# Kernel optimization log

Measured on AMD Instinct MI355X. Metric: run time of the kernel, lower is better.

Reference implementation:

```python
import jax, jax.numpy as jnp
import numpy as np

WH, WW = 7, 7           # window height/width
N = WH * WW             # tokens per window = 49
C = 768                 # num_channels
H = 24                  # num_heads
D = C // H              # head_dim = 32
B = 1024                # total windows (batch * windows-per-image)
NW = 64                 # windows per image (shift_mask leading dim)
EPS = 1e-5


def _relative_position_index():
    # Mirrors the torch buffer construction in __init__.
    coords = np.stack(np.meshgrid(np.arange(WH), np.arange(WW), indexing='ij'))  # [2,WH,WW]
    cf = coords.reshape(2, -1)                          # [2,N]
    rel = cf[:, :, None] - cf[:, None, :]               # [2,N,N]
    rel = rel.transpose(1, 2, 0).copy()                 # [N,N,2]
    rel[:, :, 0] += WH - 1
    rel[:, :, 1] += WW - 1
    rel[:, :, 0] *= 2 * WW - 1
    return jnp.asarray(rel.sum(-1), dtype=jnp.int32)    # [N,N]


def setup_inputs() -> dict:
    key = jax.random.key(0)
    ks = jax.random.split(key, 6)
    x = jax.random.normal(ks[0], (B, N, C), dtype=jnp.float32)
    shift_mask = jax.random.normal(ks[1], (NW, N, N), dtype=jnp.float32)
    w_qkv = jax.random.normal(ks[2], (3 * C, C), dtype=jnp.float32) * 0.02
    b_qkv = jnp.zeros((3 * C,), dtype=jnp.float32)
    w_proj = jax.random.normal(ks[3], (C, C), dtype=jnp.float32) * 0.02
    b_proj = jnp.zeros((C,), dtype=jnp.float32)
    rel_bias_table = jax.random.normal(ks[4], ((2 * WH - 1) * (2 * WW - 1), H), dtype=jnp.float32) * 0.02
    ln_g = jnp.ones((C,), dtype=jnp.float32)
    ln_b = jnp.zeros((C,), dtype=jnp.float32)
    rel_pos_index = _relative_position_index()
    return {
        'x': x, 'shift_mask': shift_mask,
        'w_qkv': w_qkv, 'b_qkv': b_qkv,
        'w_proj': w_proj, 'b_proj': b_proj,
        'rel_bias_table': rel_bias_table,
        'ln_g': ln_g, 'ln_b': ln_b,
        'rel_pos_index': rel_pos_index,
    }


def reference(x, shift_mask, w_qkv, b_qkv, w_proj, b_proj, rel_bias_table, ln_g, ln_b, rel_pos_index):
    B_, N_, C_ = x.shape
    # QKV projection: [B,N,3C] -> [3,B,H,N,D]
    qkv = (x @ w_qkv.T + b_qkv).reshape(B_, N_, 3, H, D).transpose(2, 0, 3, 1, 4)
    q, k, v = qkv[0], qkv[1], qkv[2]
    # Relative position bias gather: [N,N,H] -> [1,H,N,N]
    bias = rel_bias_table[rel_pos_index.reshape(-1)].reshape(N_, N_, H).transpose(2, 0, 1)[None]
    # Shift mask broadcast over batch repeats and heads: [B,1,N,N]
    mask = jnp.tile(shift_mask, (B_ // shift_mask.shape[0], 1, 1))[:, None]
    attn_bias = bias + mask  # [B,H,N,N]
    scale = 1.0 / np.sqrt(D).astype(np.float32)
    scores = jnp.einsum('bhnd,bhmd->bhnm', q, k) * scale + attn_bias
    attn = jax.nn.softmax(scores, axis=-1)
    out = jnp.einsum('bhnm,bhmd->bhnd', attn, v)       # [B,H,N,D]
    out = out.transpose(0, 2, 1, 3).reshape(B_, N_, C_)
    out = out @ w_proj.T + b_proj                      # dropout p=0 -> identity
    y = out + x
    mu = jnp.mean(y, axis=-1, keepdims=True)
    var = jnp.mean(jnp.square(y - mu), axis=-1, keepdims=True)
    return (y - mu) * jax.lax.rsqrt(var + EPS) * ln_g + ln_b
```

## Files before the change

### kernel.cpp

```cpp
#include <hip/hip_runtime.h>
#include <hip/hip_bf16.h>

#define SEQ 49
#define CH 768
#define NH 24
#define HD 32
#define NB 1024
#define NWIN 64
#define MTOT (NB*SEQ)

typedef __hip_bfloat16 bf16;
typedef __attribute__((ext_vector_type(8))) short short8;
typedef __attribute__((ext_vector_type(4))) short short4v;
typedef __attribute__((ext_vector_type(4))) float f32x4;

#define MD  ((size_t)MTOT * HD)
#define NHMD ((size_t)NH * MD)

__device__ __forceinline__ void gload16(const void* g, void* l) {
  __builtin_amdgcn_global_load_lds((__attribute__((address_space(1))) void*)g,
                                   (__attribute__((address_space(3))) void*)l,
                                   16, 0, 0);
}

__device__ __forceinline__ float bf2f(short s) {
  return __uint_as_float(((unsigned int)(unsigned short)s) << 16);
}

__global__ void cvt_bf16(const float* __restrict__ in, bf16* __restrict__ o, int n4) {
  int i = blockIdx.x * blockDim.x + threadIdx.x;
  if (i >= n4) return;
  float4 v = ((const float4*)in)[i];
  union { bf16 b[4]; short4 s; } u;
  u.b[0] = __float2bfloat16(v.x);
  u.b[1] = __float2bfloat16(v.y);
  u.b[2] = __float2bfloat16(v.z);
  u.b[3] = __float2bfloat16(v.w);
  ((short4*)o)[i] = u.s;
}

__global__ void build_comb(const float* __restrict__ table, const int* __restrict__ rpi,
                           const float* __restrict__ smask, bf16* __restrict__ comb) {
  int i = blockIdx.x * blockDim.x + threadIdx.x;
  if (i >= NWIN * NH * 1024) return;
  int idx = i * 4;
  int e0 = idx & 7;
  int l = (idx >> 3) & 63;
  int jj = (idx >> 9) & 7;
  int sh = idx >> 12;
  int h = sh % NH;
  int s = sh / NH;
  union { bf16 b[4]; short4 v; } u;
#pragma unroll
  for (int k = 0; k < 4; k++) {
    int j = jj * 8 + e0 + k;
    int mt = j >> 4, nt = (j >> 2) & 3, r = j & 3;
    int m = 16 * mt + 4 * (l >> 4) + r;
    int n = 16 * nt + (l & 15);
    float v = -1e30f;
    if (m < SEQ && n < SEQ)
      v = table[rpi[m * SEQ + n] * NH + h] + smask[s * SEQ * SEQ + m * SEQ + n];
    u.b[k] = __float2bfloat16(v);
  }
  *(short4*)(comb + idx) = u.v;
}

__global__ __launch_bounds__(512) void qkv_gemm(
    const bf16* __restrict__ A, const bf16* __restrict__ Bw,
    const float* __restrict__ bias, bf16* __restrict__ C)
{
  extern __shared__ __align__(16) bf16 lds[];
  const int tid = threadIdx.x;
  const int w = tid >> 6, l = tid & 63;
  const int lr = l & 15, lg = l >> 4;
  const int wm = w >> 2, wn = w & 3;

  const int flat = blockIdx.x;
  const int xcd = flat & 7, lid = flat >> 3;
  const int wgid = (xcd < 4 ? xcd * 221 : 884 + (xcd - 4) * 220) + lid;
  const int bm = wgid / 9, bn = wgid - 9 * bm;

  const bf16* gA[4];
  const bf16* gB[4];
  int ldst[4];
#pragma unroll
  for (int j = 0; j < 4; j++) {
    int c = j * 512 + tid;
    int row = c >> 3, cpos = c & 7;
    int srcch = cpos ^ (row & 7);
    gA[j] = A + ((size_t)(bm * 256 + row)) * CH + srcch * 8;
    gB[j] = Bw + ((size_t)(bn * 256 + row)) * CH + srcch * 8;
    ldst[j] = c * 8;
  }

  f32x4 acc[8][4];
  f32x4 zero4 = {0.f, 0.f, 0.f, 0.f};
#pragma unroll
  for (int i = 0; i < 8; i++)
#pragma unroll
    for (int j = 0; j < 4; j++) acc[i][j] = zero4;

  int offA[8][2], offB[4][2];
#pragma unroll
  for (int mi = 0; mi < 8; mi++)
#pragma unroll
    for (int ks = 0; ks < 2; ks++) {
      int rowa = wm * 128 + mi * 16 + lr;
      offA[mi][ks] = rowa * 64 + ((lg + 4 * ks) ^ (rowa & 7)) * 8;
    }
#pragma unroll
  for (int nj = 0; nj < 4; nj++)
#pragma unroll
    for (int ks = 0; ks < 2; ks++) {
      int rowb = wn * 64 + nj * 16 + lr;
      offB[nj][ks] = rowb * 64 + ((lg + 4 * ks) ^ (rowb & 7)) * 8;
    }

#pragma unroll
  for (int j = 0; j < 4; j++) gload16(gA[j], lds + ldst[j]);
#pragma unroll
  for (int j = 0; j < 4; j++) gload16(gB[j], lds + 32768 + ldst[j]);

  for (int t = 0; t < 12; ++t) {
    const int cur = t & 1;
    if (t < 11) {
      const int kk = (t + 1) * 64;
      bf16* nA = lds + (cur ^ 1) * 16384;
      bf16* nB = lds + 32768 + (cur ^ 1) * 16384;
#pragma unroll
      for (int j = 0; j < 4; j++) gload16(gA[j] + kk, nA + ldst[j]);
#pragma unroll
      for (int j = 0; j < 4; j++) gload16(gB[j] + kk, nB + ldst[j]);
      asm volatile("s_waitcnt vmcnt(8)" ::: "memory");
    } else {
      asm volatile("s_waitcnt vmcnt(0)" ::: "memory");
    }
    __builtin_amdgcn_sched_barrier(0);
    __builtin_amdgcn_s_barrier();
    __builtin_amdgcn_sched_barrier(0);
    const bf16* cA = lds + cur * 16384;
    const bf16* cB = lds + 32768 + cur * 16384;
#pragma unroll
    for (int ks = 0; ks < 2; ks++) {
      short8 af[8], bfv[4];
#pragma unroll
      for (int mi = 0; mi < 8; mi++) af[mi] = *(const short8*)(cA + offA[mi][ks]);
#pragma unroll
      for (int nj = 0; nj < 4; nj++) bfv[nj] = *(const short8*)(cB + offB[nj][ks]);
      __builtin_amdgcn_s_setprio(1);
#pragma unroll
      for (int mi = 0; mi < 8; mi++)
#pragma unroll
        for (int nj = 0; nj < 4; nj++)
          acc[mi][nj] = __builtin_amdgcn_mfma_f32_16x16x32_bf16(af[mi], bfv[nj], acc[mi][nj], 0, 0, 0);
      __builtin_amdgcn_s_setprio(0);
    }
    asm volatile("s_waitcnt lgkmcnt(0)" ::: "memory");
    __builtin_amdgcn_sched_barrier(0);
    __builtin_amdgcn_s_barrier();
    __builtin_amdgcn_sched_barrier(0);
  }

  const float scale = 0.17677669529663687f;
  const int colbase = bn * 256 + 64 * wn;
  const int rowbase = bm * 256 + 128 * wm;
#pragma unroll
  for (int nj = 0; nj < 4; nj++) {
    const int cb16 = colbase + 16 * nj;
    const int sec = cb16 / 768;
    const int rem = cb16 - sec * 768;
    const int h = rem >> 5;
    const int dbase = rem & 31;
    float bv = bias[cb16 + lr];
    if (sec == 2) {
      const size_t vbase = 2 * NHMD + ((size_t)h * HD + dbase + lr) * MTOT;
#pragma unroll
      for (int mi = 0; mi < 8; mi++) {
        size_t row = rowbase + 16 * mi + 4 * lg;
        union { bf16 b[4]; short4 s; } u;
#pragma unroll
        for (int r = 0; r < 4; r++) u.b[r] = __float2bfloat16(acc[mi][nj][r] + bv);
        *(short4*)(C + vbase + row) = u.s;
      }
    } else {
      const float mul = (sec == 0) ? scale : 1.0f;
      const size_t base = (size_t)sec * NHMD + (size_t)h * MD + dbase + lr;
#pragma unroll
      for (int mi = 0; mi < 8; mi++) {
#pragma unroll
        for (int r = 0; r < 4; r++) {
          size_t row = rowbase + 16 * mi + 4 * lg + r;
          C[base + row * HD] = __float2bfloat16((acc[mi][nj][r] + bv) * mul);
        }
      }
    }
  }
}

__global__ __launch_bounds__(256) void attn_kernel(
    const bf16* __restrict__ qkvT, const bf16* __restrict__ comb,
    bf16* __restrict__ aout)
{
  __shared__ __align__(16) bf16 P[4][64 * 72];
  const int tid = threadIdx.x;
  const int w = tid >> 6, l = tid & 63;
  const int lr = l & 15, lg = l >> 4;
  const int b = blockIdx.x;
  const int h = blockIdx.y * 4 + w;
  const size_t rowb = (size_t)b * SEQ;
  f32x4 zero4 = {0.f, 0.f, 0.f, 0.f};

  const bf16* qb = qkvT + (size_t)h * MD + rowb * HD;
  const bf16* kb = qkvT + NHMD + (size_t)h * MD + rowb * HD;
  const bf16* vT = qkvT + 2 * NHMD + (size_t)h * HD * MTOT;

  short8 qf[4], kf[4];
#pragma unroll
  for (int mt = 0; mt < 4; mt++)
    qf[mt] = *(const short8*)(qb + (16 * mt + lr) * HD + 8 * lg);
#pragma unroll
  for (int nt = 0; nt < 4; nt++)
    kf[nt] = *(const short8*)(kb + (16 * nt + lr) * HD + 8 * lg);

  f32x4 s[4][4];
#pragma unroll
  for (int mt = 0; mt < 4; mt++)
#pragma unroll
    for (int nt = 0; nt < 4; nt++)
      s[mt][nt] = __builtin_amdgcn_mfma_f32_16x16x32_bf16(qf[mt], kf[nt], zero4, 0, 0, 0);

  short8 pb[2][2];
#pragma unroll
  for (int kt = 0; kt < 2; kt++)
#pragma unroll
    for (int dt = 0; dt < 2; dt++)
      pb[kt][dt] = *(const short8*)(vT + ((size_t)(16 * dt + lr)) * MTOT + rowb + 32 * kt + 8 * lg);

  const bf16* cbp = comb + (((size_t)(b & (NWIN - 1)) * NH + h) << 12);
  short8 c8[8];
#pragma unroll
  for (int jj = 0; jj < 8; jj++)
    c8[jj] = *(const short8*)(cbp + (jj * 64 + l) * 8);
#pragma unroll
  for (int jj = 0; jj < 8; jj++)
#pragma unroll
    for (int e = 0; e < 8; e++)
      s[jj >> 1][(jj & 1) * 2 + (e >> 2)][e & 3] += bf2f(c8[jj][e]);

  float inv[4][4];
#pragma unroll
  for (int mt = 0; mt < 4; mt++)
#pragma unroll
    for (int r = 0; r < 4; r++) {
      float t = 0.f;
#pragma unroll
      for (int nt = 0; nt < 4; nt++) {
        float e = __expf(s[mt][nt][r]);
        s[mt][nt][r] = e;
        t += e;
      }
      t += __shfl_xor(t, 1, 64);
      t += __shfl_xor(t, 2, 64);
      t += __shfl_xor(t, 4, 64);
      t += __shfl_xor(t, 8, 64);
      inv[mt][r] = 1.0f / t;
    }

#pragma unroll
  for (int mt = 0; mt < 4; mt++)
#pragma unroll
    for (int nt = 0; nt < 4; nt++)
#pragma unroll
      for (int r = 0; r < 4; r++)
        P[w][(16 * mt + 4 * lg + r) * 72 + 16 * nt + lr] =
            __float2bfloat16(s[mt][nt][r]);

  f32x4 o[4][2];
#pragma unroll
  for (int mt = 0; mt < 4; mt++) { o[mt][0] = zero4; o[mt][1] = zero4; }
#pragma unroll
  for (int kt = 0; kt < 2; kt++) {
    short8 pa[4];
#pragma unroll
    for (int mt = 0; mt < 4; mt++)
      pa[mt] = *(const short8*)(&P[w][(16 * mt + lr) * 72 + 32 * kt + 8 * lg]);
#pragma unroll
    for (int mt = 0; mt < 4; mt++)
#pragma unroll
      for (int dt = 0; dt < 2; dt++)
        o[mt][dt] = __builtin_amdgcn_mfma_f32_16x16x32_bf16(pa[mt], pb[kt][dt], o[mt][dt], 0, 0, 0);
  }

#pragma unroll
  for (int mt = 0; mt < 4; mt++)
#pragma unroll
    for (int dt = 0; dt < 2; dt++)
#pragma unroll
      for (int r = 0; r < 4; r++) {
        int m = 16 * mt + 4 * lg + r;
        if (m < SEQ)
          aout[(rowb + m) * CH + h * HD + 16 * dt + lr] =
              __float2bfloat16(o[mt][dt][r] * inv[mt][r]);
      }
}

__global__ __launch_bounds__(256) void proj_gemm(
    const bf16* __restrict__ A, const bf16* __restrict__ Bw,
    const float* __restrict__ bias, const float* __restrict__ x,
    bf16* __restrict__ Y)
{
  __shared__ __align__(16) bf16 As[2 * 128 * 64];
  __shared__ __align__(16) bf16 Bs[2 * 128 * 64];
  const int tid = threadIdx.x;
  const int w = tid >> 6, l = tid & 63;
  const int lr = l & 15, lg = l >> 4;
  const int wm = w >> 1, wn = w & 1;

  const int flat = blockIdx.x;
  const int wg = (flat & 7) * 294 + (flat >> 3);
  const int bm = wg / 6, bn = wg - 6 * (wg / 6);

  const bf16* gA[4];
  const bf16* gB[4];
  int ldst[4];
#pragma unroll
  for (int j = 0; j < 4; j++) {
    int c = j * 256 + tid;
    int row = c >> 3, cpos = c & 7;
    int srcch = cpos ^ (row & 7);
    gA[j] = A + ((size_t)(bm * 128 + row)) * CH + srcch * 8;
    gB[j] = Bw + ((size_t)(bn * 128 + row)) * CH + srcch * 8;
    ldst[j] = c * 8;
  }

  f32x4 acc[4][4];
  f32x4 zero4 = {0.f, 0.f, 0.f, 0.f};
#pragma unroll
  for (int i = 0; i < 4; i++)
#pragma unroll
    for (int j = 0; j < 4; j++) acc[i][j] = zero4;

  int offA[4][2], offB[4][2];
#pragma unroll
  for (int mi = 0; mi < 4; mi++) {
#pragma unroll
    for (int ks = 0; ks < 2; ks++) {
      int rowa = 64 * wm + 16 * mi + lr;
      offA[mi][ks] = rowa * 64 + ((lg + 4 * ks) ^ (rowa & 7)) * 8;
      int rowb = 64 * wn + 16 * mi + lr;
      offB[mi][ks] = rowb * 64 + ((lg + 4 * ks) ^ (rowb & 7)) * 8;
    }
  }

#pragma unroll
  for (int j = 0; j < 4; j++) gload16(gA[j], As + ldst[j]);
#pragma unroll
  for (int j = 0; j < 4; j++) gload16(gB[j], Bs + ldst[j]);
#pragma unroll
  for (int j = 0; j < 4; j++) gload16(gA[j] + 64, As + 8192 + ldst[j]);
#pragma unroll
  for (int j = 0; j < 4; j++) gload16(gB[j] + 64, Bs + 8192 + ldst[j]);

  for (int t = 0; t < 12; ++t) {
    if (t < 11) asm volatile("s_waitcnt vmcnt(8)" ::: "memory");
    else        asm volatile("s_waitcnt vmcnt(0)" ::: "memory");
    __builtin_amdgcn_sched_barrier(0);
    __builtin_amdgcn_s_barrier();
    const int base = (t & 1) * 8192;
    const bf16* cA = As + base;
    const bf16* cB = Bs + base;
    short8 af[4][2], bfv[4][2];
#pragma unroll
    for (int mi = 0; mi < 4; mi++)
#pragma unroll
      for (int ks = 0; ks < 2; ks++) {
        af[mi][ks] = *(const short8*)(cA + offA[mi][ks]);
        bfv[mi][ks] = *(const short8*)(cB + offB[mi][ks]);
      }
    asm volatile("s_waitcnt lgkmcnt(0)" ::: "memory");
    __builtin_amdgcn_sched_barrier(0);
    __builtin_amdgcn_s_barrier();
    if (t < 10) {
      const int kk = (t + 2) * 64;
#pragma unroll
      for (int j = 0; j < 4; j++) gload16(gA[j] + kk, As + base + ldst[j]);
#pragma unroll
      for (int j = 0; j < 4; j++) gload16(gB[j] + kk, Bs + base + ldst[j]);
    }
    __builtin_amdgcn_s_setprio(1);
#pragma unroll
    for (int ks = 0; ks < 2; ks++)
#pragma unroll
      for (int mi = 0; mi < 4; mi++)
#pragma unroll
        for (int nj = 0; nj < 4; nj++)
          acc[mi][nj] = __builtin_amdgcn_mfma_f32_16x16x32_bf16(af[mi][ks], bfv[nj][ks], acc[mi][nj], 0, 0, 0);
    __builtin_amdgcn_s_setprio(0);
  }

  const int colbase = bn * 128 + 64 * wn;
  const int rowbase = bm * 128 + 64 * wm;
#pragma unroll
  for (int nj = 0; nj < 4; nj++) {
    int col = colbase + 16 * nj + lr;
    float bv = bias[col];
#pragma unroll
    for (int mi = 0; mi < 4; mi++) {
#pragma unroll
      for (int r = 0; r < 4; r++) {
        size_t row = rowbase + 16 * mi + 4 * lg + r;
        float v = acc[mi][nj][r] + bv + x[row * CH + col];
        Y[row * CH + col] = __float2bfloat16(v);
      }
    }
  }
}

__global__ __launch_bounds__(256) void ln_kernel(
    const bf16* __restrict__ Y, const float* __restrict__ g,
    const float* __restrict__ be, float* __restrict__ out)
{
  const int w = threadIdx.x >> 6, l = threadIdx.x & 63;
  const size_t r = (size_t)blockIdx.x * 4 + w;
  const bf16* yr = Y + r * CH;

  short8 a = *(const short8*)(yr + 8 * l);
  short4v b4 = *(const short4v*)(yr + 512 + 4 * l);
  float v[12];
#pragma unroll
  for (int j = 0; j < 8; j++) v[j] = bf2f(a[j]);
#pragma unroll
  for (int j = 0; j < 4; j++) v[8 + j] = bf2f(b4[j]);

  float s1 = 0.f, s2 = 0.f;
#pragma unroll
  for (int j = 0; j < 12; j++) { s1 += v[j]; s2 += v[j] * v[j]; }
#pragma unroll
  for (int m = 1; m <= 32; m <<= 1) {
    s1 += __shfl_xor(s1, m, 64);
    s2 += __shfl_xor(s2, m, 64);
  }
  float mu = s1 * (1.0f / 768.0f);
  float var = s2 * (1.0f / 768.0f) - mu * mu;
  float rs = rsqrtf(var + 1e-5f);

  float4 g0 = *(const float4*)(g + 8 * l);
  float4 g1 = *(const float4*)(g + 8 * l + 4);
  float4 g2 = *(const float4*)(g + 512 + 4 * l);
  float4 b0 = *(const float4*)(be + 8 * l);
  float4 b1 = *(const float4*)(be + 8 * l + 4);
  float4 b2 = *(const float4*)(be + 512 + 4 * l);

  float4 o0, o1, o2;
  o0.x = (v[0] - mu) * rs * g0.x + b0.x;
  o0.y = (v[1] - mu) * rs * g0.y + b0.y;
  o0.z = (v[2] - mu) * rs * g0.z + b0.z;
  o0.w = (v[3] - mu) * rs * g0.w + b0.w;
  o1.x = (v[4] - mu) * rs * g1.x + b1.x;
  o1.y = (v[5] - mu) * rs * g1.y + b1.y;
  o1.z = (v[6] - mu) * rs * g1.z + b1.z;
  o1.w = (v[7] - mu) * rs * g1.w + b1.w;
  o2.x = (v[8] - mu) * rs * g2.x + b2.x;
  o2.y = (v[9] - mu) * rs * g2.y + b2.y;
  o2.z = (v[10] - mu) * rs * g2.z + b2.z;
  o2.w = (v[11] - mu) * rs * g2.w + b2.w;

  float* orow = out + r * CH;
  *(float4*)(orow + 8 * l) = o0;
  *(float4*)(orow + 8 * l + 4) = o1;
  *(float4*)(orow + 512 + 4 * l) = o2;
}

extern "C" void kernel_launch(void* const* d_in, const int* in_sizes, int n_in,
                              void* d_out, int out_size, void* d_ws, size_t ws_size,
                              hipStream_t stream) {
  (void)in_sizes; (void)n_in; (void)out_size; (void)ws_size;
  const float* x     = (const float*)d_in[0];
  const float* smask = (const float*)d_in[1];
  const float* wqkv  = (const float*)d_in[2];
  const float* bqkv  = (const float*)d_in[3];
  const float* wproj = (const float*)d_in[4];
  const float* bproj = (const float*)d_in[5];
  const float* table = (const float*)d_in[6];
  const float* lng   = (const float*)d_in[7];
  const float* lnb   = (const float*)d_in[8];
  const int*   rpi   = (const int*)d_in[9];
  float* out = (float*)d_out;

  char* ws = (char*)d_ws;
  bf16*  xb   = (bf16*)(ws);
  bf16*  wqb  = (bf16*)(ws + 77070336);
  bf16*  wpb  = (bf16*)(ws + 80609280);
  bf16*  comb = (bf16*)(ws + 81788928);
  bf16*  qkvT = (bf16*)(ws + 94371840);
  bf16*  aout = (bf16*)(ws);
  bf16*  yb   = (bf16*)(ws + 94371840);

  cvt_bf16<<<37632, 256, 0, stream>>>(x, xb, 9633792);
  cvt_bf16<<<1728, 256, 0, stream>>>(wqkv, wqb, 442368);
  cvt_bf16<<<576, 256, 0, stream>>>(wproj, wpb, 147456);
  build_comb<<<6144, 256, 0, stream>>>(table, rpi, smask, comb);
  qkv_gemm<<<1764, 512, 131072, stream>>>(xb, wqb, bqkv, qkvT);
  attn_kernel<<<dim3(1024, 6), 256, 0, stream>>>(qkvT, comb, aout);
  proj_gemm<<<2352, 256, 0, stream>>>(aout, wpb, bproj, x, yb);
  ln_kernel<<<12544, 256, 0, stream>>>(yb, lng, lnb, out);
}
```

Before: 548.0 us.

## Interleave prefetch with MFMA in both GEMMs and read bf16 residual in proj

Both the qkv and proj GEMM main loops now issue the next tile's global-to-LDS loads in chunks spread between the LDS fragment reads and the MFMA groups. This replaces the separate prefetch phase and the second per-iteration barrier. proj_gemm drops its prefetch-two-ahead scheme for a single-ahead double buffer. The residual add now reads the bf16 copy of x instead of fp32, which halves that traffic but lowers residual precision. aout moves to its own workspace region so xb is not overwritten before proj reads it.

```diff
diff --git a/kernel.cpp b/kernel.cpp
--- a/kernel.cpp
+++ b/kernel.cpp
@@ -123,42 +123,43 @@
 
   for (int t = 0; t < 12; ++t) {
     const int cur = t & 1;
-    if (t < 11) {
-      const int kk = (t + 1) * 64;
-      bf16* nA = lds + (cur ^ 1) * 16384;
-      bf16* nB = lds + 32768 + (cur ^ 1) * 16384;
-#pragma unroll
-      for (int j = 0; j < 4; j++) gload16(gA[j] + kk, nA + ldst[j]);
-#pragma unroll
-      for (int j = 0; j < 4; j++) gload16(gB[j] + kk, nB + ldst[j]);
-      asm volatile("s_waitcnt vmcnt(8)" ::: "memory");
-    } else {
-      asm volatile("s_waitcnt vmcnt(0)" ::: "memory");
-    }
+    asm volatile("s_waitcnt vmcnt(0)" ::: "memory");
     __builtin_amdgcn_sched_barrier(0);
     __builtin_amdgcn_s_barrier();
     __builtin_amdgcn_sched_barrier(0);
     const bf16* cA = lds + cur * 16384;
     const bf16* cB = lds + 32768 + cur * 16384;
+    bf16* nA = lds + (cur ^ 1) * 16384;
+    bf16* nB = lds + 32768 + (cur ^ 1) * 16384;
+    const int kk = (t + 1) * 64;
+    const bool pf = (t < 11);
 #pragma unroll
     for (int ks = 0; ks < 2; ks++) {
-      short8 af[8], bfv[4];
-#pragma unroll
-      for (int mi = 0; mi < 8; mi++) af[mi] = *(const short8*)(cA + offA[mi][ks]);
+      short8 bfv[4];
 #pragma unroll
       for (int nj = 0; nj < 4; nj++) bfv[nj] = *(const short8*)(cB + offB[nj][ks]);
-      __builtin_amdgcn_s_setprio(1);
-#pragma unroll
-      for (int mi = 0; mi < 8; mi++)
-#pragma unroll
-        for (int nj = 0; nj < 4; nj++)
-          acc[mi][nj] = __builtin_amdgcn_mfma_f32_16x16x32_bf16(af[mi], bfv[nj], acc[mi][nj], 0, 0, 0);
-      __builtin_amdgcn_s_setprio(0);
-    }
-    asm volatile("s_waitcnt lgkmcnt(0)" ::: "memory");
-    __builtin_amdgcn_sched_barrier(0);
-    __builtin_amdgcn_s_barrier();
-    __builtin_amdgcn_sched_barrier(0);
+#pragma unroll
+      for (int hp = 0; hp < 2; hp++) {
+        short8 af[4];
+#pragma unroll
+        for (int mi = 0; mi < 4; mi++) af[mi] = *(const short8*)(cA + offA[hp * 4 + mi][ks]);
+        if (pf) {
+          const int j = ks * 2 + hp;
+          gload16(gA[j] + kk, nA + ldst[j]);
+          gload16(gB[j] + kk, nB + ldst[j]);
+        }
+        asm volatile("s_waitcnt lgkmcnt(0)" ::: "memory");
+        __builtin_amdgcn_sched_barrier(0);
+        __builtin_amdgcn_s_setprio(1);
+#pragma unroll
+        for (int mi = 0; mi < 4; mi++)
+#pragma unroll
+          for (int nj = 0; nj < 4; nj++)
+            acc[hp * 4 + mi][nj] =
+                __builtin_amdgcn_mfma_f32_16x16x32_bf16(af[mi], bfv[nj], acc[hp * 4 + mi][nj], 0, 0, 0);
+        __builtin_amdgcn_s_setprio(0);
+      }
+    }
   }
 
   const float scale = 0.17677669529663687f;
@@ -306,7 +307,7 @@
 
 __global__ __launch_bounds__(256) void proj_gemm(
     const bf16* __restrict__ A, const bf16* __restrict__ Bw,
-    const float* __restrict__ bias, const float* __restrict__ x,
+    const float* __restrict__ bias, const bf16* __restrict__ xb,
     bf16* __restrict__ Y)
 {
   __shared__ __align__(16) bf16 As[2 * 128 * 64];
@@ -356,46 +357,44 @@
   for (int j = 0; j < 4; j++) gload16(gA[j], As + ldst[j]);
 #pragma unroll
   for (int j = 0; j < 4; j++) gload16(gB[j], Bs + ldst[j]);
-#pragma unroll
-  for (int j = 0; j < 4; j++) gload16(gA[j] + 64, As + 8192 + ldst[j]);
-#pragma unroll
-  for (int j = 0; j < 4; j++) gload16(gB[j] + 64, Bs + 8192 + ldst[j]);
 
   for (int t = 0; t < 12; ++t) {
-    if (t < 11) asm volatile("s_waitcnt vmcnt(8)" ::: "memory");
-    else        asm volatile("s_waitcnt vmcnt(0)" ::: "memory");
+    const int base = (t & 1) * 8192;
+    asm volatile("s_waitcnt vmcnt(0)" ::: "memory");
     __builtin_amdgcn_sched_barrier(0);
     __builtin_amdgcn_s_barrier();
-    const int base = (t & 1) * 8192;
+    __builtin_amdgcn_sched_barrier(0);
     const bf16* cA = As + base;
     const bf16* cB = Bs + base;
-    short8 af[4][2], bfv[4][2];
-#pragma unroll
-    for (int mi = 0; mi < 4; mi++)
-#pragma unroll
-      for (int ks = 0; ks < 2; ks++) {
-        af[mi][ks] = *(const short8*)(cA + offA[mi][ks]);
-        bfv[mi][ks] = *(const short8*)(cB + offB[mi][ks]);
-      }
-    asm volatile("s_waitcnt lgkmcnt(0)" ::: "memory");
-    __builtin_amdgcn_sched_barrier(0);
-    __builtin_amdgcn_s_barrier();
-    if (t < 10) {
-      const int kk = (t + 2) * 64;
-#pragma unroll
-      for (int j = 0; j < 4; j++) gload16(gA[j] + kk, As + base + ldst[j]);
-#pragma unroll
-      for (int j = 0; j < 4; j++) gload16(gB[j] + kk, Bs + base + ldst[j]);
-    }
-    __builtin_amdgcn_s_setprio(1);
-#pragma unroll
-    for (int ks = 0; ks < 2; ks++)
+    bf16* nA = As + (base ^ 8192);
+    bf16* nB = Bs + (base ^ 8192);
+    const int kk = (t + 1) * 64;
+    const bool pf = (t < 11);
+#pragma unroll
+    for (int ks = 0; ks < 2; ks++) {
+      short8 af[4], bfv[4];
+#pragma unroll
+      for (int mi = 0; mi < 4; mi++) {
+        af[mi] = *(const short8*)(cA + offA[mi][ks]);
+        bfv[mi] = *(const short8*)(cB + offB[mi][ks]);
+      }
+      if (pf) {
+#pragma unroll
+        for (int j = 0; j < 2; j++) {
+          gload16(gA[ks * 2 + j] + kk, nA + ldst[ks * 2 + j]);
+          gload16(gB[ks * 2 + j] + kk, nB + ldst[ks * 2 + j]);
+        }
+      }
+      asm volatile("s_waitcnt lgkmcnt(0)" ::: "memory");
+      __builtin_amdgcn_sched_barrier(0);
+      __builtin_amdgcn_s_setprio(1);
 #pragma unroll
       for (int mi = 0; mi < 4; mi++)
 #pragma unroll
         for (int nj = 0; nj < 4; nj++)
-          acc[mi][nj] = __builtin_amdgcn_mfma_f32_16x16x32_bf16(af[mi][ks], bfv[nj][ks], acc[mi][nj], 0, 0, 0);
-    __builtin_amdgcn_s_setprio(0);
+          acc[mi][nj] = __builtin_amdgcn_mfma_f32_16x16x32_bf16(af[mi], bfv[nj], acc[mi][nj], 0, 0, 0);
+      __builtin_amdgcn_s_setprio(0);
+    }
   }
 
   const int colbase = bn * 128 + 64 * wn;
@@ -409,7 +408,7 @@
 #pragma unroll
       for (int r = 0; r < 4; r++) {
         size_t row = rowbase + 16 * mi + 4 * lg + r;
-        float v = acc[mi][nj][r] + bv + x[row * CH + col];
+        float v = acc[mi][nj][r] + bv + bf2f(((const short*)xb)[row * CH + col]);
         Y[row * CH + col] = __float2bfloat16(v);
       }
     }
@@ -493,7 +492,7 @@
   bf16*  wpb  = (bf16*)(ws + 80609280);
   bf16*  comb = (bf16*)(ws + 81788928);
   bf16*  qkvT = (bf16*)(ws + 94371840);
-  bf16*  aout = (bf16*)(ws);
+  bf16*  aout = (bf16*)(ws + 325582848);
   bf16*  yb   = (bf16*)(ws + 94371840);
 
   cvt_bf16<<<37632, 256, 0, stream>>>(x, xb, 9633792);
@@ -502,6 +501,6 @@
   build_comb<<<6144, 256, 0, stream>>>(table, rpi, smask, comb);
   qkv_gemm<<<1764, 512, 131072, stream>>>(xb, wqb, bqkv, qkvT);
   attn_kernel<<<dim3(1024, 6), 256, 0, stream>>>(qkvT, comb, aout);
-  proj_gemm<<<2352, 256, 0, stream>>>(aout, wpb, bproj, x, yb);
+  proj_gemm<<<2352, 256, 0, stream>>>(aout, wpb, bproj, xb, yb);
   ln_kernel<<<12544, 256, 0, stream>>>(yb, lng, lnb, out);
 }
```

New measurement: 542.9 us. Within noise of the previous version (-0.9%).
